# Kernel tuning notes

Measured on AMD Instinct MI355X. Metric: run time of the kernel, lower is better.

Reference implementation:

```python
import jax, jax.numpy as jnp
import numpy as np
import math

B, L, DIN, DOUT = 4, 1024, 64, 10
D, N = 512, 16            # hidden_dim (d_model), state_dim (d_state)
R = math.ceil(D / 16)     # dt_rank = 32
DT_MIN, DT_MAX = 1e-3, 1e-1


def _mamba_params(key):
    k1, k2, k3 = jax.random.split(key, 3)
    xproj_w = jax.random.normal(k1, (R + 2 * N, D), jnp.float32) * (D ** -0.5)
    dt_std = R ** -0.5
    dtproj_w = jax.random.uniform(k2, (D, R), jnp.float32, -dt_std, dt_std)
    dt = jnp.exp(jax.random.uniform(k3, (D,), jnp.float32)
                 * (math.log(DT_MAX) - math.log(DT_MIN)) + math.log(DT_MIN))
    dt = jnp.clip(dt, 1e-4, None)
    dtproj_b = dt + jnp.log(-jnp.expm1(-dt))          # inverse softplus
    A_log = jnp.log(jnp.broadcast_to(jnp.arange(1, N + 1, dtype=jnp.float32), (D, N)))
    Dp = jnp.ones((D,), jnp.float32)
    return xproj_w, dtproj_w, dtproj_b, A_log, Dp


def setup_inputs() -> dict:
    key = jax.random.key(0)
    ks = jax.random.split(key, 8)
    inp = {
        'x': jax.random.normal(ks[0], (B, L, DIN), jnp.float32),
        'W_in': jax.random.normal(ks[1], (D, DIN), jnp.float32) * (DIN ** -0.5),
        'b_in': jnp.zeros((D,), jnp.float32),
        'mix1_w': jax.random.normal(ks[2], (D, D), jnp.float32) * (D ** -0.5),
        'mix1_b': jnp.zeros((D,), jnp.float32),
        'mix2_w': jax.random.normal(ks[3], (D, D), jnp.float32) * (D ** -0.5),
        'mix2_b': jnp.zeros((D,), jnp.float32),
        'out_w': jax.random.normal(ks[4], (DOUT, D), jnp.float32) * (D ** -0.5),
        'out_b': jnp.zeros((DOUT,), jnp.float32),
    }
    (inp['m1_xproj'], inp['m1_dtw'], inp['m1_dtb'], inp['m1_Alog'], inp['m1_D']) = _mamba_params(ks[5])
    (inp['m2_xproj'], inp['m2_dtw'], inp['m2_dtb'], inp['m2_Alog'], inp['m2_D']) = _mamba_params(ks[6])
    return inp


def mamba_block(h, xproj_w, dtproj_w, dtproj_b, A_log, Dp):
    # h: (b, l, d) ; selective scan with A = -exp(A_log), delta_softplus=True
    b, l, d = h.shape
    A = -jnp.exp(A_log)                              # (d, n)
    x_dbl = jnp.einsum('bld,rd->blr', h, xproj_w)    # (b, l, r+2n)
    dt, Bm, Cm = jnp.split(x_dbl, [R, R + N], axis=-1)
    delta = jax.nn.softplus(jnp.einsum('blr,dr->bld', dt, dtproj_w) + dtproj_b)  # (b,l,d)
    dA = jnp.exp(delta[..., None] * A)                               # (b,l,d,n)
    dBu = delta[..., None] * Bm[:, :, None, :] * h[..., None]        # (b,l,d,n)

    def step(hstate, inp_t):
        dA_t, dBu_t, C_t = inp_t                     # (b,d,n),(b,d,n),(b,n)
        hstate = dA_t * hstate + dBu_t
        y = jnp.einsum('bdn,bn->bd', hstate, C_t)
        return hstate, y

    h0 = jnp.zeros((b, d, N), h.dtype)
    _, ys = jax.lax.scan(step, h0,
                         (jnp.swapaxes(dA, 0, 1), jnp.swapaxes(dBu, 0, 1), jnp.swapaxes(Cm, 0, 1)))
    y = jnp.swapaxes(ys, 0, 1) + h * Dp              # (b, l, d)
    return y


def reference(x, W_in, b_in, m1_xproj, m1_dtw, m1_dtb, m1_Alog, m1_D,
              mix1_w, mix1_b, m2_xproj, m2_dtw, m2_dtb, m2_Alog, m2_D,
              mix2_w, mix2_b, out_w, out_b):
    h = jnp.einsum('bli,di->bld', x, W_in) + b_in
    y = h
    h = mamba_block(h, m1_xproj, m1_dtw, m1_dtb, m1_Alog, m1_D)
    h = jax.nn.gelu(h, approximate=False)
    h = jnp.einsum('bld,ed->ble', h, mix1_w) + mix1_b
    h = h + y
    y = h
    h = mamba_block(h, m2_xproj, m2_dtw, m2_dtb, m2_Alog, m2_D)
    h = jax.nn.gelu(h, approximate=False)
    h = jnp.einsum('bld,ed->ble', h, mix2_w) + mix2_b
    h = h + y
    h = h.mean(axis=1)                               # (b, d)
    return jnp.einsum('bd,od->bo', h, out_w) + out_b
```

## Files before the change

### kernel.cpp

```cpp
#include <hip/hip_runtime.h>
#include <math.h>

typedef unsigned short ushort_t;
typedef short bf8_t __attribute__((ext_vector_type(8)));
typedef float f4_t  __attribute__((ext_vector_type(4)));

constexpr int B_   = 4;
constexpr int L_   = 1024;
constexpr int DIN_ = 64;
constexpr int DOUT_= 10;
constexpr int D_   = 512;
constexpr int N_   = 16;
constexpr int R_   = 32;
constexpr int RN_  = 64;
constexpr int M_   = B_ * L_;

constexpr int CN_ = 64;
constexpr int CL_ = L_ / CN_;

__device__ float    g_h   [M_ * D_];
__device__ float    g_h2  [M_ * D_];
__device__ ushort_t g_hbf [M_ * D_];
__device__ ushort_t g_gelubf[M_ * D_];
__device__ float    g_stL  [B_ * CN_ * D_ * N_];
__device__ float    g_sumd [B_ * CN_ * D_];
__device__ float    g_carry[B_ * CN_ * D_ * N_];
__device__ float    g_mean [B_ * D_];
__device__ ushort_t g_w1bf [D_ * D_];
__device__ ushort_t g_w2bf [D_ * D_];
__device__ ushort_t g_xp1bf[RN_ * D_];
__device__ ushort_t g_xp2bf[RN_ * D_];

__device__ __forceinline__ float gelu_f(float x) {
  return 0.5f * x * (1.0f + erff(x * 0.7071067811865475f));
}
__device__ __forceinline__ float softplus_f(float x) {
  return fmaxf(x, 0.0f) + log1pf(__expf(-fabsf(x)));
}
__device__ __forceinline__ ushort_t f2bf(float x) {
  union { float f; unsigned u; } v; v.f = x;
  unsigned r = v.u + 0x7fffu + ((v.u >> 16) & 1u);
  return (ushort_t)(r >> 16);
}

__device__ __forceinline__ void in_mfma_part(int bx,
                                             const float* __restrict__ x,
                                             const float* __restrict__ w,
                                             const float* __restrict__ bias) {
  __shared__ ushort_t As[64][72];
  __shared__ ushort_t Bs[64][72];
  const int tid  = threadIdx.x;
  const int m0   = (bx >> 3) * 64;
  const int n0   = (bx & 7) * 64;
  const int lane = tid & 63;
  const int wv   = tid >> 6;
  const int quad = lane >> 4;
  const int ln   = lane & 15;
  const int mw   = (wv & 1) * 32;
  const int nw   = (wv >> 1) * 32;

  {
    const int m = tid >> 2, q = (tid & 3) << 4;
#pragma unroll
    for (int i = 0; i < 4; ++i) {
      float4 va = *(const float4*)&x[(size_t)(m0 + m) * 64 + q + i * 4];
      float4 vb = *(const float4*)&w[(size_t)(n0 + m) * 64 + q + i * 4];
      ushort4 oa, ob;
      oa.x = f2bf(va.x); oa.y = f2bf(va.y); oa.z = f2bf(va.z); oa.w = f2bf(va.w);
      ob.x = f2bf(vb.x); ob.y = f2bf(vb.y); ob.z = f2bf(vb.z); ob.w = f2bf(vb.w);
      *(ushort4*)&As[m][q + i * 4] = oa;
      *(ushort4*)&Bs[m][q + i * 4] = ob;
    }
  }
  __syncthreads();

  f4_t acc[2][2] = {};
#pragma unroll
  for (int k1 = 0; k1 < 64; k1 += 32) {
    bf8_t a0 = *(const bf8_t*)&As[mw +      ln][k1 + quad * 8];
    bf8_t a1 = *(const bf8_t*)&As[mw + 16 + ln][k1 + quad * 8];
    bf8_t b0 = *(const bf8_t*)&Bs[nw +      ln][k1 + quad * 8];
    bf8_t b1 = *(const bf8_t*)&Bs[nw + 16 + ln][k1 + quad * 8];
    acc[0][0] = __builtin_amdgcn_mfma_f32_16x16x32_bf16(a0, b0, acc[0][0], 0, 0, 0);
    acc[0][1] = __builtin_amdgcn_mfma_f32_16x16x32_bf16(a0, b1, acc[0][1], 0, 0, 0);
    acc[1][0] = __builtin_amdgcn_mfma_f32_16x16x32_bf16(a1, b0, acc[1][0], 0, 0, 0);
    acc[1][1] = __builtin_amdgcn_mfma_f32_16x16x32_bf16(a1, b1, acc[1][1], 0, 0, 0);
  }

  float bj[2] = { bias[n0 + nw + ln], bias[n0 + nw + 16 + ln] };
#pragma unroll
  for (int i = 0; i < 2; ++i)
#pragma unroll
    for (int j = 0; j < 2; ++j) {
      const int nc = n0 + nw + 16 * j + ln;
#pragma unroll
      for (int r = 0; r < 4; ++r) {
        const int row = m0 + mw + 16 * i + quad * 4 + r;
        const size_t idx = (size_t)row * D_ + nc;
        float v = acc[i][j][r] + bj[j];
        g_h[idx] = v;
        g_hbf[idx] = f2bf(v);
      }
    }
}

__global__ __launch_bounds__(256) void k_pre(const float* __restrict__ x,
                                             const float* __restrict__ w_in,
                                             const float* __restrict__ b_in,
                                             const float* __restrict__ w1,
                                             const float* __restrict__ w2,
                                             const float* __restrict__ xp1,
                                             const float* __restrict__ xp2) {
  const int bx = blockIdx.x;
  if (bx < 512) { in_mfma_part(bx, x, w_in, b_in); return; }
  if (bx == 1088) {
#pragma unroll
    for (int j = 0; j < 8; ++j) g_mean[threadIdx.x * 8 + j] = 0.0f;
    return;
  }
  int i = ((bx - 512) * 256 + threadIdx.x) * 4;
  const float* src; ushort_t* dst; int off;
  if (i < 262144)      { src = w1;  dst = g_w1bf;  off = i; }
  else if (i < 524288) { src = w2;  dst = g_w2bf;  off = i - 262144; }
  else if (i < 557056) { src = xp1; dst = g_xp1bf; off = i - 524288; }
  else                 { src = xp2; dst = g_xp2bf; off = i - 557056; }
  float4 v = *(const float4*)&src[off];
  ushort4 o; o.x = f2bf(v.x); o.y = f2bf(v.y); o.z = f2bf(v.z); o.w = f2bf(v.w);
  *(ushort4*)&dst[off] = o;
}

template<bool DUAL, bool MEAN>
__device__ __forceinline__ void gemm_bf16_dev(
    const ushort_t* __restrict__ Abf, const ushort_t* __restrict__ Wbf,
    const float* __restrict__ bias, const float* __restrict__ res,
    float* __restrict__ out, ushort_t* __restrict__ obf) {
  __shared__ ushort_t As[64][72];
  __shared__ ushort_t Bs[64][72];
  const int tid  = threadIdx.x;
  const int m0   = (blockIdx.x >> 3) * 64;
  const int n0   = (blockIdx.x & 7) * 64;
  const int lane = tid & 63;
  const int wv   = tid >> 6;
  const int quad = lane >> 4;
  const int ln   = lane & 15;
  const int mw   = (wv & 1) * 32;
  const int nw   = (wv >> 1) * 32;

  f4_t acc[2][2] = {};

  for (int k0 = 0; k0 < 512; k0 += 64) {
#pragma unroll
    for (int c = 0; c < 2; ++c) {
      int idx = tid + c * 256;
      int m = idx >> 3, kq = (idx & 7) << 3;
      *(float4*)&As[m][kq] = *(const float4*)&Abf[(size_t)(m0 + m) * 512 + k0 + kq];
      *(float4*)&Bs[m][kq] = *(const float4*)&Wbf[(size_t)(n0 + m) * 512 + k0 + kq];
    }
    __syncthreads();
#pragma unroll
    for (int k1 = 0; k1 < 64; k1 += 32) {
      bf8_t a0 = *(const bf8_t*)&As[mw +      ln][k1 + quad * 8];
      bf8_t a1 = *(const bf8_t*)&As[mw + 16 + ln][k1 + quad * 8];
      bf8_t b0 = *(const bf8_t*)&Bs[nw +      ln][k1 + quad * 8];
      bf8_t b1 = *(const bf8_t*)&Bs[nw + 16 + ln][k1 + quad * 8];
      acc[0][0] = __builtin_amdgcn_mfma_f32_16x16x32_bf16(a0, b0, acc[0][0], 0, 0, 0);
      acc[0][1] = __builtin_amdgcn_mfma_f32_16x16x32_bf16(a0, b1, acc[0][1], 0, 0, 0);
      acc[1][0] = __builtin_amdgcn_mfma_f32_16x16x32_bf16(a1, b0, acc[1][0], 0, 0, 0);
      acc[1][1] = __builtin_amdgcn_mfma_f32_16x16x32_bf16(a1, b1, acc[1][1], 0, 0, 0);
    }
    __syncthreads();
  }

  float bj[2] = { bias[n0 + nw + ln], bias[n0 + nw + 16 + ln] };
  float psum[2][2] = {{0.f, 0.f}, {0.f, 0.f}};
#pragma unroll
  for (int i = 0; i < 2; ++i)
#pragma unroll
    for (int j = 0; j < 2; ++j) {
      const int nc = n0 + nw + 16 * j + ln;
#pragma unroll
      for (int r = 0; r < 4; ++r) {
        const int row = m0 + mw + 16 * i + quad * 4 + r;
        const size_t idx = (size_t)row * D_ + nc;
        float v = acc[i][j][r] + bj[j] + res[idx];
        out[idx] = v;
        if constexpr (DUAL) obf[idx] = f2bf(v);
        if constexpr (MEAN) psum[i][j] += v;
      }
    }
  if constexpr (MEAN) {
    __shared__ float ssum[16][64];
#pragma unroll
    for (int i = 0; i < 2; ++i)
#pragma unroll
      for (int j = 0; j < 2; ++j) {
        const int rg = (wv & 1) * 8 + i * 4 + quad;
        const int cl = (wv >> 1) * 32 + j * 16 + ln;
        ssum[rg][cl] = psum[i][j];
      }
    __syncthreads();
    if (tid < 64) {
      float s = 0.f;
#pragma unroll
      for (int rg = 0; rg < 16; ++rg) s += ssum[rg][tid];
      const int b = m0 >> 10;
      atomicAdd(&g_mean[b * D_ + n0 + tid], s);
    }
  }
}

__global__ __launch_bounds__(256) void k_mix1g(const float* __restrict__ bias) {
  gemm_bf16_dev<true, false>(g_gelubf, g_w1bf, bias, g_h, g_h2, g_hbf);
}
__global__ __launch_bounds__(256) void k_mix2g(const float* __restrict__ bias) {
  gemm_bf16_dev<false, true>(g_gelubf, g_w2bf, bias, g_h2, g_h, nullptr);
}

__global__ __launch_bounds__(512) void k_finalB(const float* out_w, const float* out_b,
                                                float* out) {
  __shared__ float sm[D_];
  __shared__ float sp[DOUT_ * 16];
  const int b = blockIdx.x, tid = threadIdx.x;
  sm[tid] = g_mean[b * D_ + tid] * (1.0f / L_);
  __syncthreads();
  if (tid < DOUT_ * 16) {
    int o = tid >> 4, seg = tid & 15;
    float p = 0.0f;
#pragma unroll
    for (int i = 0; i < 32; ++i)
      p += sm[seg * 32 + i] * out_w[o * D_ + seg * 32 + i];
    sp[tid] = p;
  }
  __syncthreads();
  if (tid < DOUT_) {
    float v = out_b[tid];
#pragma unroll
    for (int i = 0; i < 16; ++i) v += sp[tid * 16 + i];
    out[b * DOUT_ + tid] = v;
  }
}

__device__ __forceinline__ void load_A(const float* __restrict__ Alog, int d,
                                       float* A) {
#pragma unroll
  for (int n = 0; n < 16; n += 4) {
    float4 t = *(const float4*)&Alog[d * N_ + n];
    A[n + 0] = -__expf(t.x); A[n + 1] = -__expf(t.y);
    A[n + 2] = -__expf(t.z); A[n + 3] = -__expf(t.w);
  }
}

__device__ __forceinline__ void xdbl_tile(const ushort_t* __restrict__ xpbf,
                                          int row0, int tid,
                                          ushort_t (*As)[520], float (*sx)[65]) {
  const int lane = tid & 63;
  const int wv   = tid >> 6;
  const int quad = lane >> 4;
  const int ln   = lane & 15;
#pragma unroll
  for (int i = 0; i < 2; ++i) {
    int idx = tid + i * 512;
    int m = idx >> 6, kq = (idx & 63) << 3;
    *(float4*)&As[m][kq] = *(const float4*)&g_hbf[(size_t)(row0 + m) * 512 + kq];
  }
  __syncthreads();
  if (wv < 4) {
    f4_t acc = {};
#pragma unroll
    for (int k0 = 0; k0 < 512; k0 += 32) {
      bf8_t a  = *(const bf8_t*)&As[ln][k0 + quad * 8];
      bf8_t bb = *(const bf8_t*)&xpbf[(size_t)(wv * 16 + ln) * 512 + k0 + quad * 8];
      acc = __builtin_amdgcn_mfma_f32_16x16x32_bf16(a, bb, acc, 0, 0, 0);
    }
#pragma unroll
    for (int r = 0; r < 4; ++r)
      sx[quad * 4 + r][wv * 16 + ln] = acc[r];
  }
  __syncthreads();
}

__device__ __forceinline__ void p1f_dev(const float* __restrict__ h,
                                        const ushort_t* __restrict__ xpbf,
                                        const float* __restrict__ dtw,
                                        const float* __restrict__ dtb,
                                        const float* __restrict__ Alog) {
  __shared__ ushort_t As[16][520];
  __shared__ float    sx[16][65];
  const int tid  = threadIdx.x;
  const int c    = blockIdx.x & (CN_ - 1);
  const int b    = blockIdx.x >> 6;
  const int row0 = b * L_ + c * CL_;
  const int d    = tid;

  float w[32];
#pragma unroll
  for (int r = 0; r < 32; r += 4) {
    float4 t = *(const float4*)&dtw[d * R_ + r];
    w[r] = t.x; w[r + 1] = t.y; w[r + 2] = t.z; w[r + 3] = t.w;
  }
  const float bias = dtb[d];
  float A[16];
  load_A(Alog, d, A);

  xdbl_tile(xpbf, row0, tid, As, sx);

  float st[16] = {};
  float sumd = 0.0f;
#pragma unroll
  for (int l = 0; l < CL_; ++l) {
    float acc2 = bias;
#pragma unroll
    for (int k = 0; k < 32; ++k) acc2 = fmaf(sx[l][k], w[k], acc2);
    const float delta = softplus_f(acc2);
    const float dh = delta * h[(size_t)(row0 + l) * D_ + d];
    sumd += delta;
#pragma unroll
    for (int n = 0; n < 16; ++n) {
      float dA = __expf(delta * A[n]);
      st[n] = fmaf(dA, st[n], dh * sx[l][32 + n]);
    }
  }
  const size_t o = ((size_t)(b * CN_ + c) * D_ + d) * N_;
#pragma unroll
  for (int n = 0; n < 16; n += 4)
    *(float4*)&g_stL[o + n] = make_float4(st[n], st[n+1], st[n+2], st[n+3]);
  g_sumd[(b * CN_ + c) * D_ + d] = sumd;
}

__global__ __launch_bounds__(512, 4) void k_p1f_1(const float* dtw, const float* dtb,
                                                  const float* Alog) {
  p1f_dev(g_h, g_xp1bf, dtw, dtb, Alog);
}
__global__ __launch_bounds__(512, 4) void k_p1f_2(const float* dtw, const float* dtb,
                                                  const float* Alog) {
  p1f_dev(g_h2, g_xp2bf, dtw, dtb, Alog);
}

__global__ __launch_bounds__(256) void k_scan_carry(const float* __restrict__ Alog) {
  const int g = blockIdx.x * 256 + threadIdx.x;
  const int n = g & 15;
  const int d = (g >> 4) & (D_ - 1);
  const int b = g >> 13;
  const float A = -__expf(Alog[d * N_ + n]);
  float carry = 0.0f;
#pragma unroll
  for (int c0 = 0; c0 < CN_; c0 += 16) {
    float s[16], p[16];
#pragma unroll
    for (int j = 0; j < 16; ++j) {
      s[j] = g_stL[((size_t)(b * CN_ + c0 + j) * D_ + d) * N_ + n];
      p[j] = g_sumd[(b * CN_ + c0 + j) * D_ + d];
    }
#pragma unroll
    for (int j = 0; j < 16; ++j) {
      g_carry[((size_t)(b * CN_ + c0 + j) * D_ + d) * N_ + n] = carry;
      carry = fmaf(__expf(A * p[j]), carry, s[j]);
    }
  }
}

__device__ __forceinline__ void p2f_dev(const float* __restrict__ h,
                                        const ushort_t* __restrict__ xpbf,
                                        const float* __restrict__ dtw,
                                        const float* __restrict__ dtb,
                                        const float* __restrict__ Alog,
                                        const float* __restrict__ Dp,
                                        ushort_t* __restrict__ ybf) {
  __shared__ ushort_t As[16][520];
  __shared__ float    sx[16][65];
  const int tid  = threadIdx.x;
  const int c    = blockIdx.x & (CN_ - 1);
  const int b    = blockIdx.x >> 6;
  const int row0 = b * L_ + c * CL_;
  const int d    = tid;

  float w[32];
#pragma unroll
  for (int r = 0; r < 32; r += 4) {
    float4 t = *(const float4*)&dtw[d * R_ + r];
    w[r] = t.x; w[r + 1] = t.y; w[r + 2] = t.z; w[r + 3] = t.w;
  }
  const float bias = dtb[d];
  float A[16];
  load_A(Alog, d, A);
  const float Dpv = Dp[d];

  xdbl_tile(xpbf, row0, tid, As, sx);

  float st[16];
  const size_t o = ((size_t)(b * CN_ + c) * D_ + d) * N_;
#pragma unroll
  for (int n = 0; n < 16; n += 4) {
    float4 t = *(const float4*)&g_carry[o + n];
    st[n] = t.x; st[n+1] = t.y; st[n+2] = t.z; st[n+3] = t.w;
  }
#pragma unroll
  for (int l = 0; l < CL_; ++l) {
    float acc2 = bias;
#pragma unroll
    for (int k = 0; k < 32; ++k) acc2 = fmaf(sx[l][k], w[k], acc2);
    const float delta = softplus_f(acc2);
    const float hv = h[(size_t)(row0 + l) * D_ + d];
    const float dh = delta * hv;
    float y = 0.0f;
#pragma unroll
    for (int n = 0; n < 16; ++n) {
      float dA = __expf(delta * A[n]);
      st[n] = fmaf(dA, st[n], dh * sx[l][32 + n]);
      y = fmaf(st[n], sx[l][48 + n], y);
    }
    ybf[(size_t)(row0 + l) * D_ + d] = f2bf(gelu_f(y + hv * Dpv));
  }
}

__global__ __launch_bounds__(512, 4) void k_p2f_1(const float* dtw, const float* dtb,
                                                  const float* Alog, const float* Dp) {
  p2f_dev(g_h, g_xp1bf, dtw, dtb, Alog, Dp, g_gelubf);
}
__global__ __launch_bounds__(512, 4) void k_p2f_2(const float* dtw, const float* dtb,
                                                  const float* Alog, const float* Dp) {
  p2f_dev(g_h2, g_xp2bf, dtw, dtb, Alog, Dp, g_gelubf);
}

extern "C" void kernel_launch(void* const* d_in, const int* in_sizes, int n_in,
                              void* d_out, int out_size, void* d_ws, size_t ws_size,
                              hipStream_t stream) {
  const float* x        = (const float*)d_in[0];
  const float* W_in     = (const float*)d_in[1];
  const float* b_in     = (const float*)d_in[2];
  const float* mix1_w   = (const float*)d_in[3];
  const float* mix1_b   = (const float*)d_in[4];
  const float* mix2_w   = (const float*)d_in[5];
  const float* mix2_b   = (const float*)d_in[6];
  const float* out_w    = (const float*)d_in[7];
  const float* out_b    = (const float*)d_in[8];
  const float* m1_xproj = (const float*)d_in[9];
  const float* m1_dtw   = (const float*)d_in[10];
  const float* m1_dtb   = (const float*)d_in[11];
  const float* m1_Alog  = (const float*)d_in[12];
  const float* m1_D     = (const float*)d_in[13];
  const float* m2_xproj = (const float*)d_in[14];
  const float* m2_dtw   = (const float*)d_in[15];
  const float* m2_dtb   = (const float*)d_in[16];
  const float* m2_Alog  = (const float*)d_in[17];
  const float* m2_D     = (const float*)d_in[18];
  float* out = (float*)d_out;

  const int gScan  = B_ * CN_;
  const int gCarry = (B_ * D_ * N_) / 256;
  const int gMix   = (M_ / 64) * (D_ / 64);

  k_pre<<<1089, 256, 0, stream>>>(x, W_in, b_in, mix1_w, mix2_w, m1_xproj, m2_xproj);

  k_p1f_1     <<<gScan,  512, 0, stream>>>(m1_dtw, m1_dtb, m1_Alog);
  k_scan_carry<<<gCarry, 256, 0, stream>>>(m1_Alog);
  k_p2f_1     <<<gScan,  512, 0, stream>>>(m1_dtw, m1_dtb, m1_Alog, m1_D);
  k_mix1g     <<<gMix,   256, 0, stream>>>(mix1_b);
  k_p1f_2     <<<gScan,  512, 0, stream>>>(m2_dtw, m2_dtb, m2_Alog);
  k_scan_carry<<<gCarry, 256, 0, stream>>>(m2_Alog);
  k_p2f_2     <<<gScan,  512, 0, stream>>>(m2_dtw, m2_dtb, m2_Alog, m2_D);
  k_mix2g     <<<gMix,   256, 0, stream>>>(mix2_b);
  k_finalB<<<B_, 512, 0, stream>>>(out_w, out_b, out);
}
```

Before: 237.6 us.

## Fuse mix GEMM into scan phase-2 kernel, keeping GELU output in LDS

The separate bf16 mix GEMM kernels are removed. Each scan phase-2 block now writes its 16-row GELU output into shared memory and multiplies it by the mix weights with MFMA, reading weights directly from global memory. The residual add, the bf16 copy and the mean accumulation all happen in the fused epilogue. This drops one kernel launch per block and the global round-trip of the GELU activations. In exchange every block re-reads the full 512x512 weight matrix without LDS tiling, and the MFMA work now sits inside a 512-thread block capped by its launch bounds.

```diff
diff --git a/kernel.cpp b/kernel.cpp
--- a/kernel.cpp
+++ b/kernel.cpp
@@ -21,7 +21,6 @@
 __device__ float    g_h   [M_ * D_];
 __device__ float    g_h2  [M_ * D_];
 __device__ ushort_t g_hbf [M_ * D_];
-__device__ ushort_t g_gelubf[M_ * D_];
 __device__ float    g_stL  [B_ * CN_ * D_ * N_];
 __device__ float    g_sumd [B_ * CN_ * D_];
 __device__ float    g_carry[B_ * CN_ * D_ * N_];
@@ -129,93 +128,6 @@
   *(ushort4*)&dst[off] = o;
 }
 
-template<bool DUAL, bool MEAN>
-__device__ __forceinline__ void gemm_bf16_dev(
-    const ushort_t* __restrict__ Abf, const ushort_t* __restrict__ Wbf,
-    const float* __restrict__ bias, const float* __restrict__ res,
-    float* __restrict__ out, ushort_t* __restrict__ obf) {
-  __shared__ ushort_t As[64][72];
-  __shared__ ushort_t Bs[64][72];
-  const int tid  = threadIdx.x;
-  const int m0   = (blockIdx.x >> 3) * 64;
-  const int n0   = (blockIdx.x & 7) * 64;
-  const int lane = tid & 63;
-  const int wv   = tid >> 6;
-  const int quad = lane >> 4;
-  const int ln   = lane & 15;
-  const int mw   = (wv & 1) * 32;
-  const int nw   = (wv >> 1) * 32;
-
-  f4_t acc[2][2] = {};
-
-  for (int k0 = 0; k0 < 512; k0 += 64) {
-#pragma unroll
-    for (int c = 0; c < 2; ++c) {
-      int idx = tid + c * 256;
-      int m = idx >> 3, kq = (idx & 7) << 3;
-      *(float4*)&As[m][kq] = *(const float4*)&Abf[(size_t)(m0 + m) * 512 + k0 + kq];
-      *(float4*)&Bs[m][kq] = *(const float4*)&Wbf[(size_t)(n0 + m) * 512 + k0 + kq];
-    }
-    __syncthreads();
-#pragma unroll
-    for (int k1 = 0; k1 < 64; k1 += 32) {
-      bf8_t a0 = *(const bf8_t*)&As[mw +      ln][k1 + quad * 8];
-      bf8_t a1 = *(const bf8_t*)&As[mw + 16 + ln][k1 + quad * 8];
-      bf8_t b0 = *(const bf8_t*)&Bs[nw +      ln][k1 + quad * 8];
-      bf8_t b1 = *(const bf8_t*)&Bs[nw + 16 + ln][k1 + quad * 8];
-      acc[0][0] = __builtin_amdgcn_mfma_f32_16x16x32_bf16(a0, b0, acc[0][0], 0, 0, 0);
-      acc[0][1] = __builtin_amdgcn_mfma_f32_16x16x32_bf16(a0, b1, acc[0][1], 0, 0, 0);
-      acc[1][0] = __builtin_amdgcn_mfma_f32_16x16x32_bf16(a1, b0, acc[1][0], 0, 0, 0);
-      acc[1][1] = __builtin_amdgcn_mfma_f32_16x16x32_bf16(a1, b1, acc[1][1], 0, 0, 0);
-    }
-    __syncthreads();
-  }
-
-  float bj[2] = { bias[n0 + nw + ln], bias[n0 + nw + 16 + ln] };
-  float psum[2][2] = {{0.f, 0.f}, {0.f, 0.f}};
-#pragma unroll
-  for (int i = 0; i < 2; ++i)
-#pragma unroll
-    for (int j = 0; j < 2; ++j) {
-      const int nc = n0 + nw + 16 * j + ln;
-#pragma unroll
-      for (int r = 0; r < 4; ++r) {
-        const int row = m0 + mw + 16 * i + quad * 4 + r;
-        const size_t idx = (size_t)row * D_ + nc;
-        float v = acc[i][j][r] + bj[j] + res[idx];
-        out[idx] = v;
-        if constexpr (DUAL) obf[idx] = f2bf(v);
-        if constexpr (MEAN) psum[i][j] += v;
-      }
-    }
-  if constexpr (MEAN) {
-    __shared__ float ssum[16][64];
-#pragma unroll
-    for (int i = 0; i < 2; ++i)
-#pragma unroll
-      for (int j = 0; j < 2; ++j) {
-        const int rg = (wv & 1) * 8 + i * 4 + quad;
-        const int cl = (wv >> 1) * 32 + j * 16 + ln;
-        ssum[rg][cl] = psum[i][j];
-      }
-    __syncthreads();
-    if (tid < 64) {
-      float s = 0.f;
-#pragma unroll
-      for (int rg = 0; rg < 16; ++rg) s += ssum[rg][tid];
-      const int b = m0 >> 10;
-      atomicAdd(&g_mean[b * D_ + n0 + tid], s);
-    }
-  }
-}
-
-__global__ __launch_bounds__(256) void k_mix1g(const float* __restrict__ bias) {
-  gemm_bf16_dev<true, false>(g_gelubf, g_w1bf, bias, g_h, g_h2, g_hbf);
-}
-__global__ __launch_bounds__(256) void k_mix2g(const float* __restrict__ bias) {
-  gemm_bf16_dev<false, true>(g_gelubf, g_w2bf, bias, g_h2, g_h, nullptr);
-}
-
 __global__ __launch_bounds__(512) void k_finalB(const float* out_w, const float* out_b,
                                                 float* out) {
   __shared__ float sm[D_];
@@ -359,19 +271,27 @@
   }
 }
 
-__device__ __forceinline__ void p2f_dev(const float* __restrict__ h,
-                                        const ushort_t* __restrict__ xpbf,
-                                        const float* __restrict__ dtw,
-                                        const float* __restrict__ dtb,
-                                        const float* __restrict__ Alog,
-                                        const float* __restrict__ Dp,
-                                        ushort_t* __restrict__ ybf) {
+template<bool DUAL, bool MEAN>
+__device__ __forceinline__ void p2fm_dev(const float* __restrict__ h,
+                                         const ushort_t* __restrict__ xpbf,
+                                         const float* __restrict__ dtw,
+                                         const float* __restrict__ dtb,
+                                         const float* __restrict__ Alog,
+                                         const float* __restrict__ Dp,
+                                         const ushort_t* __restrict__ mixw,
+                                         const float* __restrict__ mixb,
+                                         float* __restrict__ hout,
+                                         ushort_t* __restrict__ obf) {
   __shared__ ushort_t As[16][520];
   __shared__ float    sx[16][65];
   const int tid  = threadIdx.x;
   const int c    = blockIdx.x & (CN_ - 1);
   const int b    = blockIdx.x >> 6;
   const int row0 = b * L_ + c * CL_;
+  const int lane = tid & 63;
+  const int wv   = tid >> 6;
+  const int quad = lane >> 4;
+  const int ln   = lane & 15;
   const int d    = tid;
 
   float w[32];
@@ -409,17 +329,53 @@
       st[n] = fmaf(dA, st[n], dh * sx[l][32 + n]);
       y = fmaf(st[n], sx[l][48 + n], y);
     }
-    ybf[(size_t)(row0 + l) * D_ + d] = f2bf(gelu_f(y + hv * Dpv));
-  }
-}
-
-__global__ __launch_bounds__(512, 4) void k_p2f_1(const float* dtw, const float* dtb,
-                                                  const float* Alog, const float* Dp) {
-  p2f_dev(g_h, g_xp1bf, dtw, dtb, Alog, Dp, g_gelubf);
-}
-__global__ __launch_bounds__(512, 4) void k_p2f_2(const float* dtw, const float* dtb,
-                                                  const float* Alog, const float* Dp) {
-  p2f_dev(g_h2, g_xp2bf, dtw, dtb, Alog, Dp, g_gelubf);
+    As[l][d] = f2bf(gelu_f(y + hv * Dpv));
+  }
+  __syncthreads();
+
+  f4_t acc[4] = {};
+#pragma unroll 4
+  for (int k0 = 0; k0 < 512; k0 += 32) {
+    bf8_t a = *(const bf8_t*)&As[ln][k0 + quad * 8];
+#pragma unroll
+    for (int j = 0; j < 4; ++j) {
+      bf8_t bb = *(const bf8_t*)&mixw[(size_t)(wv * 64 + j * 16 + ln) * 512 +
+                                      k0 + quad * 8];
+      acc[j] = __builtin_amdgcn_mfma_f32_16x16x32_bf16(a, bb, acc[j], 0, 0, 0);
+    }
+  }
+
+#pragma unroll
+  for (int j = 0; j < 4; ++j) {
+    const int nc = wv * 64 + j * 16 + ln;
+    const float bj = mixb[nc];
+    float msum = 0.0f;
+#pragma unroll
+    for (int r = 0; r < 4; ++r) {
+      const int row = row0 + quad * 4 + r;
+      const size_t idx = (size_t)row * D_ + nc;
+      float v = acc[j][r] + bj + h[idx];
+      hout[idx] = v;
+      if constexpr (DUAL) obf[idx] = f2bf(v);
+      if constexpr (MEAN) msum += v;
+    }
+    if constexpr (MEAN) {
+      msum += __shfl_xor(msum, 16);
+      msum += __shfl_xor(msum, 32);
+      if (quad == 0) atomicAdd(&g_mean[b * D_ + nc], msum);
+    }
+  }
+}
+
+__global__ __launch_bounds__(512, 4) void k_p2fm_1(const float* dtw, const float* dtb,
+                                                   const float* Alog, const float* Dp,
+                                                   const float* mixb) {
+  p2fm_dev<true, false>(g_h, g_xp1bf, dtw, dtb, Alog, Dp, g_w1bf, mixb, g_h2, g_hbf);
+}
+__global__ __launch_bounds__(512, 4) void k_p2fm_2(const float* dtw, const float* dtb,
+                                                   const float* Alog, const float* Dp,
+                                                   const float* mixb) {
+  p2fm_dev<false, true>(g_h2, g_xp2bf, dtw, dtb, Alog, Dp, g_w2bf, mixb, g_h, nullptr);
 }
 
 extern "C" void kernel_launch(void* const* d_in, const int* in_sizes, int n_in,
@@ -448,17 +404,14 @@
 
   const int gScan  = B_ * CN_;
   const int gCarry = (B_ * D_ * N_) / 256;
-  const int gMix   = (M_ / 64) * (D_ / 64);
 
   k_pre<<<1089, 256, 0, stream>>>(x, W_in, b_in, mix1_w, mix2_w, m1_xproj, m2_xproj);
 
   k_p1f_1     <<<gScan,  512, 0, stream>>>(m1_dtw, m1_dtb, m1_Alog);
   k_scan_carry<<<gCarry, 256, 0, stream>>>(m1_Alog);
-  k_p2f_1     <<<gScan,  512, 0, stream>>>(m1_dtw, m1_dtb, m1_Alog, m1_D);
-  k_mix1g     <<<gMix,   256, 0, stream>>>(mix1_b);
+  k_p2fm_1    <<<gScan,  512, 0, stream>>>(m1_dtw, m1_dtb, m1_Alog, m1_D, mix1_b);
   k_p1f_2     <<<gScan,  512, 0, stream>>>(m2_dtw, m2_dtb, m2_Alog);
   k_scan_carry<<<gCarry, 256, 0, stream>>>(m2_Alog);
-  k_p2f_2     <<<gScan,  512, 0, stream>>>(m2_dtw, m2_dtb, m2_Alog, m2_D);
-  k_mix2g     <<<gMix,   256, 0, stream>>>(mix2_b);
+  k_p2fm_2    <<<gScan,  512, 0, stream>>>(m2_dtw, m2_dtb, m2_Alog, m2_D, mix2_b);
   k_finalB<<<B_, 512, 0, stream>>>(out_w, out_b, out);
 }
```

Measured after the change: 241.8 us. No clear change (+1.8%).
